# Optimization experiments

Measured on AMD Instinct MI355X. Metric: run time of the kernel, lower is better.

The kernel has to match this reference:

```python
import jax, jax.numpy as jnp
import numpy as np

NEG_SLOPE = 0.2

def _gat_conv(x, src, dst, W, att_src, att_dst, bias, num_nodes):
    # x: [N, Fin], W: [H*C, Fin], att_*: [H, C], bias: [H*C]
    H, C = att_src.shape
    xh = (x @ W.T).reshape(num_nodes, H, C)            # [N,H,C]
    a_s = jnp.einsum('nhc,hc->nh', xh, att_src)         # [N,H]
    a_d = jnp.einsum('nhc,hc->nh', xh, att_dst)
    e = jax.nn.leaky_relu(a_s[src] + a_d[dst], NEG_SLOPE)  # [E,H]
    # segment softmax over destination node per head
    m = jax.ops.segment_max(e, dst, num_segments=num_nodes)      # [N,H]
    ex = jnp.exp(e - m[dst])
    s = jax.ops.segment_sum(ex, dst, num_segments=num_nodes)     # [N,H]
    alpha = ex / (s[dst] + 1e-16)                                # [E,H]
    msg = xh[src] * alpha[:, :, None]                            # [E,H,C]
    out = jax.ops.segment_sum(msg, dst, num_segments=num_nodes)  # [N,H,C]
    return out.reshape(num_nodes, H * C) + bias


def setup_inputs() -> dict:
    key = jax.random.key(0)
    ks = jax.random.split(key, 16)
    N, E, Fin, Hd, H1, G = 50000, 800000, 128, 128, 4, 128
    x = jax.random.normal(ks[0], (N, Fin), dtype=jnp.float32)
    edge_index = jax.random.randint(ks[1], (2, E), 0, N, dtype=jnp.int64)
    batch = jnp.sort(jax.random.randint(ks[2], (N,), 0, G, dtype=jnp.int64))
    sc1 = 1.0 / np.sqrt(Fin)
    sc2 = 1.0 / np.sqrt(Hd * H1)
    sch = 1.0 / np.sqrt(Hd)
    return {
        'x': x, 'edge_index': edge_index, 'batch': batch,
        'W1': jax.random.normal(ks[3], (Hd * H1, Fin), dtype=jnp.float32) * sc1,
        'as1': jax.random.normal(ks[4], (H1, Hd), dtype=jnp.float32) * 0.1,
        'ad1': jax.random.normal(ks[5], (H1, Hd), dtype=jnp.float32) * 0.1,
        'b1': jnp.zeros((Hd * H1,), dtype=jnp.float32),
        'W2': jax.random.normal(ks[6], (Hd, Hd * H1), dtype=jnp.float32) * sc2,
        'as2': jax.random.normal(ks[7], (1, Hd), dtype=jnp.float32) * 0.1,
        'ad2': jax.random.normal(ks[8], (1, Hd), dtype=jnp.float32) * 0.1,
        'b2': jnp.zeros((Hd,), dtype=jnp.float32),
        'Wh1': jax.random.normal(ks[9], (Hd, Hd), dtype=jnp.float32) * sch,
        'bh1': jnp.zeros((Hd,), dtype=jnp.float32),
        'Wh2': jax.random.normal(ks[10], (1, Hd), dtype=jnp.float32) * sch,
        'bh2': jnp.zeros((1,), dtype=jnp.float32),
    }


def reference(x, edge_index, batch, W1, as1, ad1, b1, W2, as2, ad2, b2, Wh1, bh1, Wh2, bh2):
    N = x.shape[0]
    G = 128  # num graphs
    # add self loops (PyG GATConv default)
    loops = jnp.arange(N, dtype=edge_index.dtype)
    src = jnp.concatenate([edge_index[0], loops])
    dst = jnp.concatenate([edge_index[1], loops])
    h = _gat_conv(x, src, dst, W1, as1, ad1, b1, N)   # [N, 512]
    h = jax.nn.elu(h)
    h = _gat_conv(h, src, dst, W2, as2, ad2, b2, N)   # [N, 128]
    h = jax.nn.elu(h)
    # global mean pool over batch
    sums = jax.ops.segment_sum(h, batch, num_segments=G)
    cnts = jax.ops.segment_sum(jnp.ones((N,), dtype=h.dtype), batch, num_segments=G)
    pooled = sums / jnp.maximum(cnts, 1.0)[:, None]   # [G, 128]
    z = jax.nn.relu(pooled @ Wh1.T + bh1)
    out = z @ Wh2.T + bh2                             # [G, 1]
    return out.reshape(-1)
```

## Files before the change

### kernel.cpp

```cpp
#include <hip/hip_runtime.h>
#include <cstdint>
#include <cstddef>

#define NEG_SLOPE 0.2f

typedef _Float16 f16x8 __attribute__((ext_vector_type(8)));
typedef _Float16 f16x2 __attribute__((ext_vector_type(2)));
typedef float    f32x4 __attribute__((ext_vector_type(4)));
typedef float    f32x2 __attribute__((ext_vector_type(2)));

__device__ __forceinline__ float leaky(float x){ return x > 0.f ? x : NEG_SLOPE * x; }
__device__ __forceinline__ float elu(float x){ return x > 0.f ? x : __expf(x) - 1.f; }

__global__ __launch_bounds__(256) void k_front(const float* __restrict__ W1,
                                               const float* __restrict__ W2,
                                               const float* __restrict__ as1,
                                               const float* __restrict__ ad1,
                                               _Float16* __restrict__ W1hi, _Float16* __restrict__ W1lo,
                                               _Float16* __restrict__ W2hi, _Float16* __restrict__ W2lo,
                                               float* __restrict__ w_s, float* __restrict__ w_d,
                                               const int* __restrict__ ei, int* __restrict__ deg,
                                               unsigned short* __restrict__ rank,
                                               const int* __restrict__ batch, int* __restrict__ gstart,
                                               int E, int Ep, int N, int G, int nbc)
{
    int b = blockIdx.x;
    if (b < 512) {
        const float* src = (b < 256) ? W1 : W2;
        _Float16* hi = (b < 256) ? W1hi : W2hi;
        _Float16* lo = (b < 256) ? W1lo : W2lo;
        int i = ((b & 255) << 8) + threadIdx.x;
        float v = src[i];
        _Float16 h = (_Float16)v;
        hi[i] = h;
        lo[i] = (_Float16)(v - (float)h);
    } else if (b < 514) {
        int h = (b - 512) * 2 + (threadIdx.x >> 7);
        int k = threadIdx.x & 127;
        float s = 0.f, d = 0.f;
        for (int c = 0; c < 128; ++c) {
            float w = W1[((size_t)(h * 128 + c)) * 128 + k];
            s += as1[h * 128 + c] * w;
            d += ad1[h * 128 + c] * w;
        }
        w_s[h * 128 + k] = s;
        w_d[h * 128 + k] = d;
    } else if (b < 514 + nbc) {
        int e = (b - 514) * 256 + threadIdx.x;
        if (e >= Ep) return;
        int dst = (e < E) ? ei[E + e] : (e - E);
        rank[e] = (unsigned short)atomicAdd(&deg[dst], 1);
    } else {
        int n = (b - 514 - nbc) * 256 + threadIdx.x;
        if (n >= N) return;
        int bb = batch[n];
        int prev = (n == 0) ? -1 : batch[n - 1];
        for (int g = prev + 1; g <= bb; ++g) gstart[g] = n;
        if (n == N - 1)
            for (int g = bb + 1; g <= G; ++g) gstart[g] = N;
    }
}

__global__ __launch_bounds__(1024) void k_scan_attn(const int* __restrict__ deg,
                                                    int* __restrict__ start,
                                                    int* __restrict__ sums,
                                                    int Ntot, int N, int nscan,
                                                    const float* __restrict__ x,
                                                    const float* __restrict__ w_s,
                                                    const float* __restrict__ w_d,
                                                    float* __restrict__ a_s,
                                                    float* __restrict__ a_d,
                                                    _Float16* __restrict__ xh)
{
    if ((int)blockIdx.x < nscan) {
        __shared__ int sm[1024];
        int tid = threadIdx.x;
        int i = blockIdx.x * 1024 + tid;
        int v = (i < N) ? deg[i] : 0;
        sm[tid] = v; __syncthreads();
        for (int off = 1; off < 1024; off <<= 1) {
            int t = (tid >= off) ? sm[tid - off] : 0;
            __syncthreads();
            sm[tid] += t;
            __syncthreads();
        }
        if (i < Ntot) start[i] = sm[tid] - v;
        if (tid == 1023) sums[blockIdx.x] = sm[1023];
    } else {
        int n = (blockIdx.x - nscan) * 16 + (threadIdx.x >> 6);
        if (n >= N) return;
        int lane = threadIdx.x & 63;
        float2 xv = *(const float2*)(x + (size_t)n * 128 + lane * 2);
        f16x2 hv = { (_Float16)xv.x, (_Float16)xv.y };
        *(f16x2*)(xh + (size_t)n * 128 + lane * 2) = hv;
        float ps[4], pd[4];
        #pragma unroll
        for (int h = 0; h < 4; ++h) {
            float2 sv = *(const float2*)(w_s + h * 128 + lane * 2);
            float2 dv = *(const float2*)(w_d + h * 128 + lane * 2);
            ps[h] = xv.x * sv.x + xv.y * sv.y;
            pd[h] = xv.x * dv.x + xv.y * dv.y;
        }
        #pragma unroll
        for (int h = 0; h < 4; ++h)
            for (int off = 32; off; off >>= 1) {
                ps[h] += __shfl_xor(ps[h], off);
                pd[h] += __shfl_xor(pd[h], off);
            }
        if (lane == 0) {
            *(float4*)(a_s + (size_t)n * 4) = make_float4(ps[0], ps[1], ps[2], ps[3]);
            *(float4*)(a_d + (size_t)n * 4) = make_float4(pd[0], pd[1], pd[2], pd[3]);
        }
    }
}

__global__ __launch_bounds__(1024) void k_scanC(int* __restrict__ start,
                                                const int* __restrict__ sums, int Ntot)
{
    int add = 0;
    for (int b = 0; b < (int)blockIdx.x; ++b) add += sums[b];
    int i = blockIdx.x * 1024 + threadIdx.x;
    if (i < Ntot) start[i] += add;
}

__global__ void k_fill(const int* __restrict__ ei, const int* __restrict__ start,
                       const unsigned short* __restrict__ rank,
                       unsigned short* __restrict__ csr_src, int E, int Ep)
{
    int e = blockIdx.x * blockDim.x + threadIdx.x;
    if (e >= Ep) return;
    int src, dst;
    if (e < E) { src = ei[e]; dst = ei[E + e]; } else { src = dst = e - E; }
    csr_src[start[dst] + rank[e]] = (unsigned short)src;
}

#define LSG 40
#define CP  136
template<bool FUSE_BIAS_ELU, bool FUSE_ATTN2>
__global__ __launch_bounds__(256, 2) void k_gemm_h(
    const _Float16* __restrict__ A, const _Float16* __restrict__ Bh,
    const _Float16* __restrict__ Bl, const float* __restrict__ bias,
    _Float16* __restrict__ C,
    const float* __restrict__ as2, const float* __restrict__ ad2,
    float* __restrict__ As2, float* __restrict__ Ad2,
    int M, int K, int lda, int ldb, int ldc,
    long aZ, long bZ, long cZ, long biasZ)
{
    __shared__ __align__(16) _Float16 smem[128 * CP];
    _Float16* As  = smem;
    _Float16* Bhs = smem + 128 * LSG;
    _Float16* Bls = smem + 256 * LSG;

    const _Float16* Ab  = A  + (size_t)blockIdx.z * aZ;
    const _Float16* Bhb = Bh + (size_t)blockIdx.z * bZ;
    const _Float16* Blb = Bl + (size_t)blockIdx.z * bZ;
    _Float16* Cb = C + (size_t)blockIdx.z * cZ;

    const int tid = threadIdx.x;
    const int wave = tid >> 6, lane = tid & 63;
    const int wm = wave >> 1, wn = wave & 1;
    const int quad = lane >> 4, l16 = lane & 15;
    const int m0 = blockIdx.x * 128;

    f32x4 acc[4][4] = {};

    for (int k0 = 0; k0 < K; k0 += 32) {
        #pragma unroll
        for (int q = 0; q < 2; ++q) {
            int idx = tid + q * 256;
            int row = idx >> 2, kq = idx & 3;
            int rg = m0 + row;
            f16x8 va = {};
            if (rg < M) va = *(const f16x8*)(Ab + (size_t)rg * lda + k0 + kq * 8);
            *(f16x8*)&As[row * LSG + kq * 8] = va;
            *(f16x8*)&Bhs[row * LSG + kq * 8] = *(const f16x8*)(Bhb + (size_t)row * ldb + k0 + kq * 8);
            *(f16x8*)&Bls[row * LSG + kq * 8] = *(const f16x8*)(Blb + (size_t)row * ldb + k0 + kq * 8);
        }
        __syncthreads();

        f16x8 af[4], bhf[4], blf[4];
        #pragma unroll
        for (int i = 0; i < 4; ++i) {
            int mr = wm * 64 + i * 16 + l16;
            af[i] = *(const f16x8*)&As[mr * LSG + quad * 8];
            int nr = wn * 64 + i * 16 + l16;
            bhf[i] = *(const f16x8*)&Bhs[nr * LSG + quad * 8];
            blf[i] = *(const f16x8*)&Bls[nr * LSG + quad * 8];
        }
        #pragma unroll
        for (int i = 0; i < 4; ++i)
            #pragma unroll
            for (int j = 0; j < 4; ++j) {
                acc[i][j] = __builtin_amdgcn_mfma_f32_16x16x32_f16(af[i], bhf[j], acc[i][j], 0, 0, 0);
                acc[i][j] = __builtin_amdgcn_mfma_f32_16x16x32_f16(af[i], blf[j], acc[i][j], 0, 0, 0);
            }
        __syncthreads();
    }

    #pragma unroll
    for (int j = 0; j < 4; ++j) {
        int n = wn * 64 + j * 16 + l16;
        float bb = 0.f;
        if (FUSE_BIAS_ELU) bb = bias[blockIdx.z * biasZ + n];
        #pragma unroll
        for (int i = 0; i < 4; ++i)
            #pragma unroll
            for (int r = 0; r < 4; ++r) {
                float v = acc[i][j][r];
                if (FUSE_BIAS_ELU) v = elu(v + bb);
                smem[(wm * 64 + i * 16 + quad * 4 + r) * CP + n] = (_Float16)v;
            }
    }
    __syncthreads();
    for (int c = tid; c < 2048; c += 256) {
        int row = c >> 4, col8 = (c & 15) * 8;
        int m = m0 + row;
        if (m < M)
            *(f16x8*)(Cb + (size_t)m * ldc + col8) = *(const f16x8*)&smem[row * CP + col8];
    }
    if (FUSE_ATTN2) {
        int row = tid >> 1, half = tid & 1;
        int d = m0 + row;
        float ss = 0.f, sd = 0.f;
        const _Float16* rp = &smem[row * CP + half * 64];
        #pragma unroll
        for (int c8 = 0; c8 < 8; ++c8) {
            f16x8 v = *(const f16x8*)(rp + c8 * 8);
            #pragma unroll
            for (int c = 0; c < 8; ++c) {
                float f = (float)v[c];
                int n = half * 64 + c8 * 8 + c;
                ss += f * as2[n];
                sd += f * ad2[n];
            }
        }
        ss += __shfl_xor(ss, 1);
        sd += __shfl_xor(sd, 1);
        if (half == 0 && d < M) { As2[d] = ss; Ad2[d] = sd; }
    }
}

__global__ __launch_bounds__(256) void k_gat1(const int* __restrict__ start,
                                              const unsigned short* __restrict__ csr,
                                              const float* __restrict__ a_s,
                                              const float* __restrict__ a_d,
                                              const _Float16* __restrict__ x,
                                              _Float16* __restrict__ agg, int N)
{
    int d = blockIdx.x * 16 + (threadIdx.x >> 4);
    if (d >= N) return;
    int g16 = threadIdx.x & 15;
    int beg = start[d], end = start[d + 1];
    int deg = end - beg;
    float4 ad4 = *(const float4*)(a_d + (size_t)d * 4);

    float sum0 = 0.f, sum1 = 0.f, sum2 = 0.f, sum3 = 0.f;
    f32x2 acc[4][4] = {};
    const _Float16* xb = x + g16 * 8;

    for (int base = 0; base < deg; base += 16) {
        int nch = deg - base; if (nch > 16) nch = 16;
        int s = 0;
        float e0 = 0.f, e1 = 0.f, e2 = 0.f, e3 = 0.f;
        if (g16 < nch) {
            s = csr[beg + base + g16];
            float4 as4 = *(const float4*)(a_s + (size_t)s * 4);
            e0 = __expf(leaky(as4.x + ad4.x));
            e1 = __expf(leaky(as4.y + ad4.y));
            e2 = __expf(leaky(as4.z + ad4.z));
            e3 = __expf(leaky(as4.w + ad4.w));
            sum0 += e0; sum1 += e1; sum2 += e2; sum3 += e3;
        }
        int t = 0;
        for (; t + 8 <= nch; t += 8) {
            int si[8];
            #pragma unroll
            for (int u = 0; u < 8; ++u) si[u] = __shfl(s, t + u, 16);
            f16x8 hv[8];
            #pragma unroll
            for (int u = 0; u < 8; ++u) hv[u] = *(const f16x8*)(xb + (size_t)si[u] * 128);
            #pragma unroll
            for (int u = 0; u < 8; ++u) {
                float w0 = __shfl(e0, t + u, 16), w1 = __shfl(e1, t + u, 16);
                float w2 = __shfl(e2, t + u, 16), w3 = __shfl(e3, t + u, 16);
                #pragma unroll
                for (int p = 0; p < 4; ++p) {
                    f32x2 v = { (float)hv[u][2*p], (float)hv[u][2*p+1] };
                    acc[0][p] += w0 * v;
                    acc[1][p] += w1 * v;
                    acc[2][p] += w2 * v;
                    acc[3][p] += w3 * v;
                }
            }
        }
        for (; t + 4 <= nch; t += 4) {
            int sA = __shfl(s, t, 16),     sB = __shfl(s, t + 1, 16);
            int sC = __shfl(s, t + 2, 16), sD = __shfl(s, t + 3, 16);
            f16x8 hA = *(const f16x8*)(xb + (size_t)sA * 128);
            f16x8 hB = *(const f16x8*)(xb + (size_t)sB * 128);
            f16x8 hC = *(const f16x8*)(xb + (size_t)sC * 128);
            f16x8 hD = *(const f16x8*)(xb + (size_t)sD * 128);
            float w0A = __shfl(e0, t, 16),     w1A = __shfl(e1, t, 16);
            float w2A = __shfl(e2, t, 16),     w3A = __shfl(e3, t, 16);
            float w0B = __shfl(e0, t + 1, 16), w1B = __shfl(e1, t + 1, 16);
            float w2B = __shfl(e2, t + 1, 16), w3B = __shfl(e3, t + 1, 16);
            float w0C = __shfl(e0, t + 2, 16), w1C = __shfl(e1, t + 2, 16);
            float w2C = __shfl(e2, t + 2, 16), w3C = __shfl(e3, t + 2, 16);
            float w0D = __shfl(e0, t + 3, 16), w1D = __shfl(e1, t + 3, 16);
            float w2D = __shfl(e2, t + 3, 16), w3D = __shfl(e3, t + 3, 16);
            #pragma unroll
            for (int p = 0; p < 4; ++p) {
                f32x2 vA = { (float)hA[2*p], (float)hA[2*p+1] };
                f32x2 vB = { (float)hB[2*p], (float)hB[2*p+1] };
                f32x2 vC = { (float)hC[2*p], (float)hC[2*p+1] };
                f32x2 vD = { (float)hD[2*p], (float)hD[2*p+1] };
                acc[0][p] += w0A * vA + w0B * vB + w0C * vC + w0D * vD;
                acc[1][p] += w1A * vA + w1B * vB + w1C * vC + w1D * vD;
                acc[2][p] += w2A * vA + w2B * vB + w2C * vC + w2D * vD;
                acc[3][p] += w3A * vA + w3B * vB + w3C * vC + w3D * vD;
            }
        }
        for (; t < nch; ++t) {
            int   si = __shfl(s,  t, 16);
            float w0 = __shfl(e0, t, 16);
            float w1 = __shfl(e1, t, 16);
            float w2 = __shfl(e2, t, 16);
            float w3 = __shfl(e3, t, 16);
            f16x8 hv = *(const f16x8*)(xb + (size_t)si * 128);
            #pragma unroll
            for (int p = 0; p < 4; ++p) {
                f32x2 v = { (float)hv[2*p], (float)hv[2*p+1] };
                acc[0][p] += w0 * v;
                acc[1][p] += w1 * v;
                acc[2][p] += w2 * v;
                acc[3][p] += w3 * v;
            }
        }
    }
    #pragma unroll
    for (int o = 1; o < 16; o <<= 1) {
        sum0 += __shfl_xor(sum0, o, 16); sum1 += __shfl_xor(sum1, o, 16);
        sum2 += __shfl_xor(sum2, o, 16); sum3 += __shfl_xor(sum3, o, 16);
    }
    float inv[4] = { 1.f / (sum0 + 1e-16f), 1.f / (sum1 + 1e-16f),
                     1.f / (sum2 + 1e-16f), 1.f / (sum3 + 1e-16f) };
    _Float16* o = agg + (size_t)d * 512 + g16 * 8;
    #pragma unroll
    for (int h = 0; h < 4; ++h) {
        f16x8 ov;
        #pragma unroll
        for (int p = 0; p < 4; ++p) {
            ov[2 * p]     = (_Float16)(acc[h][p].x * inv[h]);
            ov[2 * p + 1] = (_Float16)(acc[h][p].y * inv[h]);
        }
        *(f16x8*)(o + h * 128) = ov;
    }
}

__global__ __launch_bounds__(256) void k_gat2(const int* __restrict__ start,
                                              const unsigned short* __restrict__ csr,
                                              const float* __restrict__ a_s,
                                              const float* __restrict__ a_d,
                                              const _Float16* __restrict__ xh2,
                                              const float* __restrict__ b2,
                                              _Float16* __restrict__ h2, int N)
{
    int d = blockIdx.x * 16 + (threadIdx.x >> 4);
    if (d >= N) return;
    int g16 = threadIdx.x & 15;
    int beg = start[d], end = start[d + 1];
    int deg = end - beg;
    float ad = a_d[d];

    float sum = 0.f;
    f32x2 acc[4] = {};
    const _Float16* xb = xh2 + g16 * 8;

    for (int base = 0; base < deg; base += 16) {
        int nch = deg - base; if (nch > 16) nch = 16;
        int s = 0; float e = 0.f;
        if (g16 < nch) {
            s = csr[beg + base + g16];
            e = __expf(leaky(a_s[s] + ad));
            sum += e;
        }
        int t = 0;
        for (; t + 8 <= nch; t += 8) {
            int si[8];
            #pragma unroll
            for (int u = 0; u < 8; ++u) si[u] = __shfl(s, t + u, 16);
            f16x8 hv[8];
            #pragma unroll
            for (int u = 0; u < 8; ++u) hv[u] = *(const f16x8*)(xb + (size_t)si[u] * 128);
            #pragma unroll
            for (int u = 0; u < 8; ++u) {
                float w = __shfl(e, t + u, 16);
                #pragma unroll
                for (int p = 0; p < 4; ++p) {
                    f32x2 v = { (float)hv[u][2*p], (float)hv[u][2*p+1] };
                    acc[p] += w * v;
                }
            }
        }
        for (; t + 4 <= nch; t += 4) {
            int sA = __shfl(s, t, 16),     sB = __shfl(s, t + 1, 16);
            int sC = __shfl(s, t + 2, 16), sD = __shfl(s, t + 3, 16);
            f16x8 hA = *(const f16x8*)(xb + (size_t)sA * 128);
            f16x8 hB = *(const f16x8*)(xb + (size_t)sB * 128);
            f16x8 hC = *(const f16x8*)(xb + (size_t)sC * 128);
            f16x8 hD = *(const f16x8*)(xb + (size_t)sD * 128);
            float wA = __shfl(e, t, 16),     wB = __shfl(e, t + 1, 16);
            float wC = __shfl(e, t + 2, 16), wD = __shfl(e, t + 3, 16);
            #pragma unroll
            for (int p = 0; p < 4; ++p) {
                f32x2 vA = { (float)hA[2*p], (float)hA[2*p+1] };
                f32x2 vB = { (float)hB[2*p], (float)hB[2*p+1] };
                f32x2 vC = { (float)hC[2*p], (float)hC[2*p+1] };
                f32x2 vD = { (float)hD[2*p], (float)hD[2*p+1] };
                acc[p] += wA * vA + wB * vB + wC * vC + wD * vD;
            }
        }
        for (; t < nch; ++t) {
            int   si = __shfl(s, t, 16);
            float w  = __shfl(e, t, 16);
            f16x8 hv = *(const f16x8*)(xb + (size_t)si * 128);
            #pragma unroll
            for (int p = 0; p < 4; ++p) {
                f32x2 v = { (float)hv[2*p], (float)hv[2*p+1] };
                acc[p] += w * v;
            }
        }
    }
    #pragma unroll
    for (int o = 1; o < 16; o <<= 1) sum += __shfl_xor(sum, o, 16);
    float inv = 1.f / (sum + 1e-16f);
    f16x8 ov;
    #pragma unroll
    for (int p = 0; p < 4; ++p) {
        ov[2 * p]     = (_Float16)elu(acc[p].x * inv + b2[g16 * 8 + 2 * p]);
        ov[2 * p + 1] = (_Float16)elu(acc[p].y * inv + b2[g16 * 8 + 2 * p + 1]);
    }
    *(f16x8*)(h2 + (size_t)d * 128 + g16 * 8) = ov;
}

#define PCH 64
__global__ __launch_bounds__(128) void k_poolA(const _Float16* __restrict__ h2,
                                               const int* __restrict__ batch,
                                               float* __restrict__ pooled, int N)
{
    int c = threadIdx.x;
    int n0 = blockIdx.x * PCH;
    int n1 = n0 + PCH < N ? n0 + PCH : N;
    if (n0 >= N) return;
    int g = batch[n0];
    float acc = 0.f;
    for (int n = n0; n < n1; ++n) {
        int bg = batch[n];
        if (bg != g) { atomicAdd(&pooled[(size_t)g * 128 + c], acc); acc = 0.f; g = bg; }
        acc += (float)h2[(size_t)n * 128 + c];
    }
    atomicAdd(&pooled[(size_t)g * 128 + c], acc);
}

__global__ __launch_bounds__(128) void k_head(const float* __restrict__ pooled,
                                              const int* __restrict__ gstart,
                                              const float* __restrict__ Wh1,
                                              const float* __restrict__ bh1,
                                              const float* __restrict__ Wh2,
                                              const float* __restrict__ bh2,
                                              float* __restrict__ out)
{
    int g = blockIdx.x, c = threadIdx.x;
    __shared__ float p[128];
    __shared__ float red[128];
    float cf = (float)(gstart[g + 1] - gstart[g]); cf = cf > 1.f ? cf : 1.f;
    p[c] = pooled[(size_t)g * 128 + c] / cf;
    __syncthreads();
    float z = bh1[c];
    for (int k = 0; k < 128; ++k) z += p[k] * Wh1[c * 128 + k];
    z = z > 0.f ? z : 0.f;
    red[c] = z * Wh2[c];
    __syncthreads();
    for (int st = 64; st > 0; st >>= 1) { if (c < st) red[c] += red[c + st]; __syncthreads(); }
    if (c == 0) out[g] = red[0] + bh2[0];
}

extern "C" void kernel_launch(void* const* d_in, const int* in_sizes, int n_in,
                              void* d_out, int out_size, void* d_ws, size_t ws_size,
                              hipStream_t stream)
{
    const float* x   = (const float*)d_in[0];
    const int*   ei  = (const int*)d_in[1];
    const int*   bat = (const int*)d_in[2];
    const float* W1  = (const float*)d_in[3];
    const float* as1 = (const float*)d_in[4];
    const float* ad1 = (const float*)d_in[5];
    const float* b1  = (const float*)d_in[6];
    const float* W2  = (const float*)d_in[7];
    const float* as2 = (const float*)d_in[8];
    const float* ad2 = (const float*)d_in[9];
    const float* b2  = (const float*)d_in[10];
    const float* Wh1 = (const float*)d_in[11];
    const float* bh1 = (const float*)d_in[12];
    const float* Wh2 = (const float*)d_in[13];
    const float* bh2 = (const float*)d_in[14];
    float* out = (float*)d_out;

    const int N  = in_sizes[0] / 128;
    const int E  = in_sizes[1] / 2;
    const int Ep = E + N;
    const int G  = 128;
    const int nscan = (N + 1 + 1023) / 1024;

    char* w = (char*)d_ws;
    size_t off = 0;
    auto alloc = [&](size_t bytes) -> char* {
        char* p = w + off; off += (bytes + 511) & ~(size_t)511; return p;
    };
    _Float16* x_h  = (_Float16*)alloc((size_t)N * 128 * 2);
    _Float16* agg  = (_Float16*)alloc((size_t)N * 512 * 2);
    _Float16* h1   = (_Float16*)alloc((size_t)N * 512 * 2);
    _Float16* xh2h = (_Float16*)alloc((size_t)N * 128 * 2);
    _Float16* h2   = (_Float16*)alloc((size_t)N * 128 * 2);
    float*    As1  = (float*)alloc((size_t)N * 4 * 4);
    float*    Ad1  = (float*)alloc((size_t)N * 4 * 4);
    float*    As2  = (float*)alloc((size_t)N * 4);
    float*    Ad2  = (float*)alloc((size_t)N * 4);
    float*    w_s1 = (float*)alloc(512 * 4);
    float*    w_d1 = (float*)alloc(512 * 4);
    _Float16* W1hi = (_Float16*)alloc(65536 * 2);
    _Float16* W1lo = (_Float16*)alloc(65536 * 2);
    _Float16* W2hi = (_Float16*)alloc(65536 * 2);
    _Float16* W2lo = (_Float16*)alloc(65536 * 2);
    int* startb = (int*)alloc((size_t)(N + 1) * 4);
    unsigned short* csr  = (unsigned short*)alloc((size_t)Ep * 2);
    unsigned short* rank = (unsigned short*)alloc((size_t)Ep * 2);
    int* sums   = (int*)alloc(4096);
    int* gstart = (int*)alloc((size_t)(G + 1) * 4);
    char* zbase = w + off;
    int*   deg    = (int*)alloc((size_t)N * 4);
    float* pooled = (float*)alloc((size_t)G * 128 * 4);
    size_t zbytes = (size_t)((w + off) - zbase);

    hipMemsetAsync(zbase, 0, zbytes, stream);

    int nbc = (Ep + 255) / 256, nbg = (N + 255) / 256;
    k_front<<<514 + nbc + nbg, 256, 0, stream>>>(W1, W2, as1, ad1, W1hi, W1lo, W2hi, W2lo,
                                                 w_s1, w_d1, ei, deg, rank, bat, gstart,
                                                 E, Ep, N, G, nbc);
    k_scan_attn<<<nscan + (N + 15) / 16, 1024, 0, stream>>>(deg, startb, sums, N + 1, N, nscan,
                                                            x, w_s1, w_d1, As1, Ad1, x_h);
    k_scanC<<<nscan, 1024, 0, stream>>>(startb, sums, N + 1);
    k_fill<<<(Ep + 255) / 256, 256, 0, stream>>>(ei, startb, rank, csr, E, Ep);
    k_gat1<<<(N + 15) / 16, 256, 0, stream>>>(startb, csr, As1, Ad1, x_h, agg, N);
    k_gemm_h<true, false><<<dim3((N + 127) / 128, 1, 4), 256, 0, stream>>>(
        agg, W1hi, W1lo, b1, h1, nullptr, nullptr, nullptr, nullptr,
        N, 128, 512, 128, 512, 128L, 16384L, 128L, 128L);
    k_gemm_h<false, true><<<dim3((N + 127) / 128, 1, 1), 256, 0, stream>>>(
        h1, W2hi, W2lo, nullptr, xh2h, as2, ad2, As2, Ad2,
        N, 512, 512, 512, 128, 0L, 0L, 0L, 0L);
    k_gat2<<<(N + 15) / 16, 256, 0, stream>>>(startb, csr, As2, Ad2, xh2h, b2, h2, N);
    k_poolA<<<(N + PCH - 1) / PCH, 128, 0, stream>>>(h2, bat, pooled, N);
    k_head<<<G, 128, 0, stream>>>(pooled, gstart, Wh1, bh1, Wh2, bh2, out);
}
```

Before: 340.5 us.

## Fuse layer-1 per-head GEMM and layer-2 GEMM into one kernel keeping h1 in LDS

Replaces the two GEMM launches (per-head W1 projection with bias+ELU, then the W2 projection with attention logits) with one kernel. For each head it computes the 128x128 h1 tile into LDS and immediately feeds it as the A operand of the layer-2 GEMM, accumulating across heads. This removes the N x 512 fp16 h1 round trip through global memory and one launch. In exchange the grid shrinks from 4x391 blocks to 391 blocks (under two waves' worth on the CUs), so each block's work is serialized and occupancy/parallelism drops. LDS use also grows.

```diff
diff --git a/kernel.cpp b/kernel.cpp
--- a/kernel.cpp
+++ b/kernel.cpp
@@ -136,25 +136,20 @@
 
 #define LSG 40
 #define CP  136
-template<bool FUSE_BIAS_ELU, bool FUSE_ATTN2>
-__global__ __launch_bounds__(256, 2) void k_gemm_h(
-    const _Float16* __restrict__ A, const _Float16* __restrict__ Bh,
-    const _Float16* __restrict__ Bl, const float* __restrict__ bias,
-    _Float16* __restrict__ C,
+__global__ __launch_bounds__(256, 2) void k_gemm12(
+    const _Float16* __restrict__ agg,
+    const _Float16* __restrict__ W1hi, const _Float16* __restrict__ W1lo,
+    const float* __restrict__ b1,
+    const _Float16* __restrict__ W2hi, const _Float16* __restrict__ W2lo,
+    _Float16* __restrict__ xh2,
     const float* __restrict__ as2, const float* __restrict__ ad2,
-    float* __restrict__ As2, float* __restrict__ Ad2,
-    int M, int K, int lda, int ldb, int ldc,
-    long aZ, long bZ, long cZ, long biasZ)
-{
-    __shared__ __align__(16) _Float16 smem[128 * CP];
+    float* __restrict__ As2, float* __restrict__ Ad2, int M)
+{
+    __shared__ __align__(16) _Float16 smem[128 * LSG * 3 + 128 * CP];
     _Float16* As  = smem;
     _Float16* Bhs = smem + 128 * LSG;
     _Float16* Bls = smem + 256 * LSG;
-
-    const _Float16* Ab  = A  + (size_t)blockIdx.z * aZ;
-    const _Float16* Bhb = Bh + (size_t)blockIdx.z * bZ;
-    const _Float16* Blb = Bl + (size_t)blockIdx.z * bZ;
-    _Float16* Cb = C + (size_t)blockIdx.z * cZ;
+    _Float16* Ct  = smem + 384 * LSG;
 
     const int tid = threadIdx.x;
     const int wave = tid >> 6, lane = tid & 63;
@@ -162,67 +157,100 @@
     const int quad = lane >> 4, l16 = lane & 15;
     const int m0 = blockIdx.x * 128;
 
-    f32x4 acc[4][4] = {};
-
-    for (int k0 = 0; k0 < K; k0 += 32) {
+    f32x4 acc2[4][4] = {};
+
+    for (int h = 0; h < 4; ++h) {
+        f32x4 acc1[4][4] = {};
+        for (int k0 = 0; k0 < 128; k0 += 32) {
+            #pragma unroll
+            for (int q = 0; q < 2; ++q) {
+                int idx = tid + q * 256;
+                int row = idx >> 2, kq = idx & 3;
+                int rg = m0 + row;
+                f16x8 va = {};
+                if (rg < M) va = *(const f16x8*)(agg + (size_t)rg * 512 + h * 128 + k0 + kq * 8);
+                *(f16x8*)&As[row * LSG + kq * 8] = va;
+                size_t brow = (size_t)(h * 128 + row) * 128 + k0 + kq * 8;
+                *(f16x8*)&Bhs[row * LSG + kq * 8] = *(const f16x8*)(W1hi + brow);
+                *(f16x8*)&Bls[row * LSG + kq * 8] = *(const f16x8*)(W1lo + brow);
+            }
+            __syncthreads();
+            f16x8 af[4], bhf[4], blf[4];
+            #pragma unroll
+            for (int i = 0; i < 4; ++i) {
+                af[i]  = *(const f16x8*)&As [(wm * 64 + i * 16 + l16) * LSG + quad * 8];
+                bhf[i] = *(const f16x8*)&Bhs[(wn * 64 + i * 16 + l16) * LSG + quad * 8];
+                blf[i] = *(const f16x8*)&Bls[(wn * 64 + i * 16 + l16) * LSG + quad * 8];
+            }
+            #pragma unroll
+            for (int i = 0; i < 4; ++i)
+                #pragma unroll
+                for (int j = 0; j < 4; ++j) {
+                    acc1[i][j] = __builtin_amdgcn_mfma_f32_16x16x32_f16(af[i], bhf[j], acc1[i][j], 0, 0, 0);
+                    acc1[i][j] = __builtin_amdgcn_mfma_f32_16x16x32_f16(af[i], blf[j], acc1[i][j], 0, 0, 0);
+                }
+            __syncthreads();
+        }
         #pragma unroll
-        for (int q = 0; q < 2; ++q) {
-            int idx = tid + q * 256;
-            int row = idx >> 2, kq = idx & 3;
-            int rg = m0 + row;
-            f16x8 va = {};
-            if (rg < M) va = *(const f16x8*)(Ab + (size_t)rg * lda + k0 + kq * 8);
-            *(f16x8*)&As[row * LSG + kq * 8] = va;
-            *(f16x8*)&Bhs[row * LSG + kq * 8] = *(const f16x8*)(Bhb + (size_t)row * ldb + k0 + kq * 8);
-            *(f16x8*)&Bls[row * LSG + kq * 8] = *(const f16x8*)(Blb + (size_t)row * ldb + k0 + kq * 8);
+        for (int j = 0; j < 4; ++j) {
+            int n = wn * 64 + j * 16 + l16;
+            float bb = b1[h * 128 + n];
+            #pragma unroll
+            for (int i = 0; i < 4; ++i)
+                #pragma unroll
+                for (int r = 0; r < 4; ++r)
+                    Ct[(wm * 64 + i * 16 + quad * 4 + r) * CP + n] = (_Float16)elu(acc1[i][j][r] + bb);
         }
         __syncthreads();
-
-        f16x8 af[4], bhf[4], blf[4];
-        #pragma unroll
-        for (int i = 0; i < 4; ++i) {
-            int mr = wm * 64 + i * 16 + l16;
-            af[i] = *(const f16x8*)&As[mr * LSG + quad * 8];
-            int nr = wn * 64 + i * 16 + l16;
-            bhf[i] = *(const f16x8*)&Bhs[nr * LSG + quad * 8];
-            blf[i] = *(const f16x8*)&Bls[nr * LSG + quad * 8];
-        }
-        #pragma unroll
-        for (int i = 0; i < 4; ++i)
-            #pragma unroll
-            for (int j = 0; j < 4; ++j) {
-                acc[i][j] = __builtin_amdgcn_mfma_f32_16x16x32_f16(af[i], bhf[j], acc[i][j], 0, 0, 0);
-                acc[i][j] = __builtin_amdgcn_mfma_f32_16x16x32_f16(af[i], blf[j], acc[i][j], 0, 0, 0);
-            }
-        __syncthreads();
+        for (int k0 = 0; k0 < 128; k0 += 32) {
+            #pragma unroll
+            for (int q = 0; q < 2; ++q) {
+                int idx = tid + q * 256;
+                int row = idx >> 2, kq = idx & 3;
+                size_t brow = (size_t)row * 512 + h * 128 + k0 + kq * 8;
+                *(f16x8*)&Bhs[row * LSG + kq * 8] = *(const f16x8*)(W2hi + brow);
+                *(f16x8*)&Bls[row * LSG + kq * 8] = *(const f16x8*)(W2lo + brow);
+            }
+            __syncthreads();
+            f16x8 af[4], bhf[4], blf[4];
+            #pragma unroll
+            for (int i = 0; i < 4; ++i) {
+                af[i]  = *(const f16x8*)&Ct [(wm * 64 + i * 16 + l16) * CP + k0 + quad * 8];
+                bhf[i] = *(const f16x8*)&Bhs[(wn * 64 + i * 16 + l16) * LSG + quad * 8];
+                blf[i] = *(const f16x8*)&Bls[(wn * 64 + i * 16 + l16) * LSG + quad * 8];
+            }
+            #pragma unroll
+            for (int i = 0; i < 4; ++i)
+                #pragma unroll
+                for (int j = 0; j < 4; ++j) {
+                    acc2[i][j] = __builtin_amdgcn_mfma_f32_16x16x32_f16(af[i], bhf[j], acc2[i][j], 0, 0, 0);
+                    acc2[i][j] = __builtin_amdgcn_mfma_f32_16x16x32_f16(af[i], blf[j], acc2[i][j], 0, 0, 0);
+                }
+            __syncthreads();
+        }
     }
 
     #pragma unroll
     for (int j = 0; j < 4; ++j) {
         int n = wn * 64 + j * 16 + l16;
-        float bb = 0.f;
-        if (FUSE_BIAS_ELU) bb = bias[blockIdx.z * biasZ + n];
         #pragma unroll
         for (int i = 0; i < 4; ++i)
             #pragma unroll
-            for (int r = 0; r < 4; ++r) {
-                float v = acc[i][j][r];
-                if (FUSE_BIAS_ELU) v = elu(v + bb);
-                smem[(wm * 64 + i * 16 + quad * 4 + r) * CP + n] = (_Float16)v;
-            }
+            for (int r = 0; r < 4; ++r)
+                Ct[(wm * 64 + i * 16 + quad * 4 + r) * CP + n] = (_Float16)acc2[i][j][r];
     }
     __syncthreads();
     for (int c = tid; c < 2048; c += 256) {
         int row = c >> 4, col8 = (c & 15) * 8;
         int m = m0 + row;
         if (m < M)
-            *(f16x8*)(Cb + (size_t)m * ldc + col8) = *(const f16x8*)&smem[row * CP + col8];
-    }
-    if (FUSE_ATTN2) {
+            *(f16x8*)(xh2 + (size_t)m * 128 + col8) = *(const f16x8*)&Ct[row * CP + col8];
+    }
+    {
         int row = tid >> 1, half = tid & 1;
         int d = m0 + row;
         float ss = 0.f, sd = 0.f;
-        const _Float16* rp = &smem[row * CP + half * 64];
+        const _Float16* rp = &Ct[row * CP + half * 64];
         #pragma unroll
         for (int c8 = 0; c8 < 8; ++c8) {
             f16x8 v = *(const f16x8*)(rp + c8 * 8);
@@ -519,7 +547,6 @@
     };
     _Float16* x_h  = (_Float16*)alloc((size_t)N * 128 * 2);
     _Float16* agg  = (_Float16*)alloc((size_t)N * 512 * 2);
-    _Float16* h1   = (_Float16*)alloc((size_t)N * 512 * 2);
     _Float16* xh2h = (_Float16*)alloc((size_t)N * 128 * 2);
     _Float16* h2   = (_Float16*)alloc((size_t)N * 128 * 2);
     float*    As1  = (float*)alloc((size_t)N * 4 * 4);
@@ -553,12 +580,8 @@
     k_scanC<<<nscan, 1024, 0, stream>>>(startb, sums, N + 1);
     k_fill<<<(Ep + 255) / 256, 256, 0, stream>>>(ei, startb, rank, csr, E, Ep);
     k_gat1<<<(N + 15) / 16, 256, 0, stream>>>(startb, csr, As1, Ad1, x_h, agg, N);
-    k_gemm_h<true, false><<<dim3((N + 127) / 128, 1, 4), 256, 0, stream>>>(
-        agg, W1hi, W1lo, b1, h1, nullptr, nullptr, nullptr, nullptr,
-        N, 128, 512, 128, 512, 128L, 16384L, 128L, 128L);
-    k_gemm_h<false, true><<<dim3((N + 127) / 128, 1, 1), 256, 0, stream>>>(
-        h1, W2hi, W2lo, nullptr, xh2h, as2, ad2, As2, Ad2,
-        N, 512, 512, 512, 128, 0L, 0L, 0L, 0L);
+    k_gemm12<<<(N + 127) / 128, 256, 0, stream>>>(agg, W1hi, W1lo, b1, W2hi, W2lo,
+                                                  xh2h, as2, ad2, As2, Ad2, N);
     k_gat2<<<(N + 15) / 16, 256, 0, stream>>>(startb, csr, As2, Ad2, xh2h, b2, h2, N);
     k_poolA<<<(N + PCH - 1) / PCH, 128, 0, stream>>>(h2, bat, pooled, N);
     k_head<<<G, 128, 0, stream>>>(pooled, gstart, Wh1, bh1, Wh2, bh2, out);
```

Measured after the change: 331.3 us. 1.03x faster.
